# Kernel tuning notes

Measured on AMD Instinct MI355X. Metric: run time of the kernel, lower is better.

The kernel has to match this reference:

```python
import jax, jax.numpy as jnp
import numpy as np

D = 512
H = 8
DH = D // H
FF = 2048
E = 4
EPS = 1e-5


def _layernorm(x, g, b):
    mu = jnp.mean(x, axis=-1, keepdims=True)
    var = jnp.mean(jnp.square(x - mu), axis=-1, keepdims=True)
    return (x - mu) * jax.lax.rsqrt(var + EPS) * g + b


def setup_inputs() -> dict:
    key = jax.random.key(0)
    ks = jax.random.split(key, 12)
    B, T = 4, 2048
    s = 0.02
    return {
        "x": jax.random.normal(ks[0], (B, T, D), jnp.float32),
        "fourier_bias": jax.random.normal(ks[1], (B, T, T), jnp.float32) * 0.1,
        "Wk": jax.random.normal(ks[2], (D, D), jnp.float32) * s,
        "bk": jnp.zeros((D,), jnp.float32),
        "Wv": jax.random.normal(ks[3], (D, D), jnp.float32) * s,
        "bv": jnp.zeros((D,), jnp.float32),
        "Wo": jax.random.normal(ks[4], (D, D), jnp.float32) * s,
        "bo": jnp.zeros((D,), jnp.float32),
        "ln1_g": jnp.ones((D,), jnp.float32),
        "ln1_b": jnp.zeros((D,), jnp.float32),
        "Wg": jax.random.normal(ks[5], (D, E), jnp.float32) * s,
        "bg": jnp.zeros((E,), jnp.float32),
        "W1": jax.random.normal(ks[6], (E, D, FF), jnp.float32) * s,
        "b1": jnp.zeros((E, FF), jnp.float32),
        "W2": jax.random.normal(ks[7], (E, FF, D), jnp.float32) * s,
        "b2": jnp.zeros((E, D), jnp.float32),
        "ln2_g": jnp.ones((D,), jnp.float32),
        "ln2_b": jnp.zeros((D,), jnp.float32),
    }


def reference(x, fourier_bias, Wk, bk, Wv, bv, Wo, bo, ln1_g, ln1_b,
              Wg, bg, W1, b1, W2, b2, ln2_g, ln2_b):
    B, T, _ = x.shape
    # --- Fourier pairwise-bias "attention" ---
    K = (x @ Wk + bk).reshape(B, T, H, DH).transpose(0, 2, 1, 3)  # [B,H,T,Dh]
    V = (x @ Wv + bv).reshape(B, T, H, DH).transpose(0, 2, 1, 3)  # [B,H,T,Dh]
    # sum_j (K_j + fb_ij) * V_j = sum_j K_j*V_j  +  sum_j fb_ij * V_j
    kv_sum = jnp.sum(K * V, axis=2, keepdims=True)                # [B,H,1,Dh]
    fbV = jnp.einsum('bij,bhjd->bhid', fourier_bias, V)           # [B,H,T,Dh]
    wv = (kv_sum + fbV).transpose(0, 2, 1, 3).reshape(B, T, D)
    x = _layernorm(x + (wv @ Wo + bo), ln1_g, ln1_b)
    # --- MoE FFN, top-2 gating (dropout/noise inactive in eval) ---
    scores = jax.nn.softmax(x @ Wg + bg, axis=-1)                 # [B,T,E]
    vals, idx = jax.lax.top_k(scores, 2)                          # [B,T,2]
    w = (jax.nn.one_hot(idx[..., 0], E, dtype=x.dtype) * vals[..., 0:1]
         + jax.nn.one_hot(idx[..., 1], E, dtype=x.dtype) * vals[..., 1:2])  # [B,T,E]
    h = jax.nn.relu(jnp.einsum('btd,edf->btef', x, W1) + b1)      # [B,T,E,FF]
    y = jnp.einsum('btef,efd->bted', h, W2) + b2                  # [B,T,E,D]
    ff = jnp.einsum('bte,bted->btd', w, y)
    return _layernorm(x + ff, ln2_g, ln2_b)
```

## Files before the change

### kernel.cpp

```cpp
#include <hip/hip_runtime.h>
#include <stdint.h>

#define BB   4
#define TT   2048
#define DD   512
#define FFF  2048
#define NEXP 4
#define NTOK (BB*TT)
#define LNEPS 1e-5f

typedef unsigned short u16;
typedef __attribute__((ext_vector_type(8))) short bf16x8;
typedef __attribute__((ext_vector_type(4))) float f32x4;

__device__ __forceinline__ u16 f2bf(float f) {
  union { float f; unsigned u; } v; v.f = f;
  return (u16)((v.u + 0x7FFFu + ((v.u >> 16) & 1u)) >> 16);
}
__device__ __forceinline__ float bf2f(u16 h) {
  union { unsigned u; float f; } v; v.u = (unsigned)h << 16; return v.f;
}

__device__ __forceinline__ void gl2lds(const u16* g, u16* l) {
  __builtin_amdgcn_global_load_lds(
      (const __attribute__((address_space(1))) void*)g,
      (__attribute__((address_space(3))) void*)l, 16, 0, 0);
}


__global__ void split_f32_kernel(const float* __restrict__ in, u16* __restrict__ hi,
                                 u16* __restrict__ lo, int n4) {
  int i = blockIdx.x * blockDim.x + threadIdx.x;
  if (i >= n4) return;
  float4 f = ((const float4*)in)[i];
  u16 h0 = f2bf(f.x), h1 = f2bf(f.y), h2 = f2bf(f.z), h3 = f2bf(f.w);
  u16 l0 = f2bf(f.x - bf2f(h0)), l1 = f2bf(f.y - bf2f(h1));
  u16 l2 = f2bf(f.z - bf2f(h2)), l3 = f2bf(f.w - bf2f(h3));
  ((uint2*)hi)[i] = uint2{(unsigned)h0 | ((unsigned)h1 << 16), (unsigned)h2 | ((unsigned)h3 << 16)};
  ((uint2*)lo)[i] = uint2{(unsigned)l0 | ((unsigned)l1 << 16), (unsigned)l2 | ((unsigned)l3 << 16)};
}

__global__ void transpose_split3_kernel(const float* __restrict__ s0, const float* __restrict__ s1,
                                        const float* __restrict__ s2,
                                        u16* __restrict__ kvhi, u16* __restrict__ kvlo,
                                        u16* __restrict__ ohi,  u16* __restrict__ olo) {
  __shared__ float tile[32][33];
  const int z = blockIdx.z;
  const float* in = (z == 0) ? s0 : (z == 1) ? s1 : s2;
  int c0 = blockIdx.x * 32, r0 = blockIdx.y * 32;
  int tx = threadIdx.x, ty = threadIdx.y;
#pragma unroll
  for (int k = 0; k < 4; k++)
    tile[ty + 8*k][tx] = in[(size_t)(r0 + ty + 8*k) * DD + c0 + tx];
  __syncthreads();
#pragma unroll
  for (int k = 0; k < 4; k++) {
    float v = tile[tx][ty + 8*k];
    u16 h = f2bf(v);
    u16 l = f2bf(v - bf2f(h));
    const int c = c0 + ty + 8*k;
    if (z < 2) {
      size_t idx = (size_t)(2*c + z) * DD + r0 + tx;
      kvhi[idx] = h; kvlo[idx] = l;
    } else {
      size_t idx = (size_t)c * DD + r0 + tx;
      ohi[idx] = h; olo[idx] = l;
    }
  }
}

__global__ void transpose_cast_kernel(const float* __restrict__ in, u16* __restrict__ out,
                                      int R, int C) {
  __shared__ float tile[32][33];
  int z = blockIdx.z;
  in  += (size_t)z * R * C;
  out += (size_t)z * R * C;
  int c0 = blockIdx.x * 32, r0 = blockIdx.y * 32;
  int tx = threadIdx.x, ty = threadIdx.y;
#pragma unroll
  for (int k = 0; k < 4; k++)
    tile[ty + 8*k][tx] = in[(size_t)(r0 + ty + 8*k) * C + c0 + tx];
  __syncthreads();
#pragma unroll
  for (int k = 0; k < 4; k++)
    out[(size_t)(c0 + ty + 8*k) * R + r0 + tx] = f2bf(tile[tx][ty + 8*k]);
}

template<int MODE>
__global__ __launch_bounds__(256)
void gemm_split2_kernel(const u16* __restrict__ Ahi, const u16* __restrict__ Alo,
                        const u16* __restrict__ Bhi, const u16* __restrict__ Blo,
                        const float* __restrict__ bias0, const float* __restrict__ bias1,
                        float* __restrict__ out0,
                        u16* __restrict__ outh, u16* __restrict__ outl,
                        int M, int N, int K,
                        long long sA, long long sB, long long sO) {
  constexpr int NBUF = (MODE == 2) ? 2 : 1;
  __shared__ u16 AhL[NBUF][128*32], AlL[NBUF][128*32];
  __shared__ u16 BhL[NBUF][64*32],  BlL[NBUF][64*32];

  int mt, nt, z;
  if constexpr (MODE == 2) {
    const int gid = blockIdx.x;
    const int xcd = gid & 7, slot = gid >> 3;
    z  = xcd >> 1;
    mt = (xcd & 1) + 2 * (slot >> 3);
    nt = slot & 7;
  } else {
    mt = blockIdx.x; nt = blockIdx.y; z = blockIdx.z;
  }
  const int m0 = mt * 128, n0 = nt * 64;

  Ahi += (size_t)z * sA; Alo += (size_t)z * sA;
  Bhi += (size_t)z * sB; Blo += (size_t)z * sB;
  const int tid = threadIdx.x;
  const int lane = tid & 63, wave = tid >> 6;
  const int wm = wave >> 1, wn = wave & 1;
  const int quad = lane >> 4, l16 = lane & 15;
  const int sxor = ((l16 >> 1) & 3) << 3;

  const int ar1 = tid >> 2;
  const int ac1 = (((tid & 3) ^ ((tid >> 3) & 3)) << 3);
  const u16* pAh1 = Ahi + (size_t)(m0 + ar1) * K + ac1;
  const u16* pAh2 = Ahi + (size_t)(m0 + ar1 + 64) * K + ac1;
  const u16* pAl1 = Alo + (size_t)(m0 + ar1) * K + ac1;
  const u16* pAl2 = Alo + (size_t)(m0 + ar1 + 64) * K + ac1;
  const u16* pBh1 = Bhi + (size_t)(n0 + ar1) * K + ac1;
  const u16* pBl1 = Blo + (size_t)(n0 + ar1) * K + ac1;
  const int wofs = wave * 512;

  f32x4 acc[4][2];
#pragma unroll
  for (int i = 0; i < 4; i++)
#pragma unroll
    for (int j = 0; j < 2; j++)
      acc[i][j] = f32x4{0.f, 0.f, 0.f, 0.f};

  const int NIT = K >> 5;
  if constexpr (MODE == 2) {
    gl2lds(pAh1, &AhL[0][wofs]); gl2lds(pAh2, &AhL[0][2048 + wofs]);
    gl2lds(pAl1, &AlL[0][wofs]); gl2lds(pAl2, &AlL[0][2048 + wofs]);
    gl2lds(pBh1, &BhL[0][wofs]); gl2lds(pBl1, &BlL[0][wofs]);
    for (int it = 0; it < NIT; it++) {
      const int buf = it & 1;
      __syncthreads();
      if (it + 1 < NIT) {
        const int ko = (it + 1) << 5;
        gl2lds(pAh1 + ko, &AhL[buf ^ 1][wofs]); gl2lds(pAh2 + ko, &AhL[buf ^ 1][2048 + wofs]);
        gl2lds(pAl1 + ko, &AlL[buf ^ 1][wofs]); gl2lds(pAl2 + ko, &AlL[buf ^ 1][2048 + wofs]);
        gl2lds(pBh1 + ko, &BhL[buf ^ 1][wofs]); gl2lds(pBl1 + ko, &BlL[buf ^ 1][wofs]);
      }
      bf16x8 afh[4], afl[4], bqh[2], bql[2];
#pragma unroll
      for (int i = 0; i < 4; i++) {
        afh[i] = *(const bf16x8*)&AhL[buf][(wm*64 + i*16 + l16) * 32 + (quad*8 ^ sxor)];
        afl[i] = *(const bf16x8*)&AlL[buf][(wm*64 + i*16 + l16) * 32 + (quad*8 ^ sxor)];
      }
#pragma unroll
      for (int j = 0; j < 2; j++) {
        bqh[j] = *(const bf16x8*)&BhL[buf][(wn*32 + j*16 + l16) * 32 + (quad*8 ^ sxor)];
        bql[j] = *(const bf16x8*)&BlL[buf][(wn*32 + j*16 + l16) * 32 + (quad*8 ^ sxor)];
      }
#pragma unroll
      for (int i = 0; i < 4; i++)
#pragma unroll
        for (int j = 0; j < 2; j++) {
          acc[i][j] = __builtin_amdgcn_mfma_f32_16x16x32_bf16(afh[i], bqh[j], acc[i][j], 0, 0, 0);
          acc[i][j] = __builtin_amdgcn_mfma_f32_16x16x32_bf16(afh[i], bql[j], acc[i][j], 0, 0, 0);
          acc[i][j] = __builtin_amdgcn_mfma_f32_16x16x32_bf16(afl[i], bqh[j], acc[i][j], 0, 0, 0);
        }
    }
  } else {
    for (int it = 0; it < NIT; it++) {
      const int ko = it << 5;
      __syncthreads();
      gl2lds(pAh1 + ko, &AhL[0][wofs]); gl2lds(pAh2 + ko, &AhL[0][2048 + wofs]);
      gl2lds(pAl1 + ko, &AlL[0][wofs]); gl2lds(pAl2 + ko, &AlL[0][2048 + wofs]);
      gl2lds(pBh1 + ko, &BhL[0][wofs]); gl2lds(pBl1 + ko, &BlL[0][wofs]);
      __syncthreads();
      bf16x8 afh[4], afl[4], bqh[2], bql[2];
#pragma unroll
      for (int i = 0; i < 4; i++) {
        afh[i] = *(const bf16x8*)&AhL[0][(wm*64 + i*16 + l16) * 32 + (quad*8 ^ sxor)];
        afl[i] = *(const bf16x8*)&AlL[0][(wm*64 + i*16 + l16) * 32 + (quad*8 ^ sxor)];
      }
#pragma unroll
      for (int j = 0; j < 2; j++) {
        bqh[j] = *(const bf16x8*)&BhL[0][(wn*32 + j*16 + l16) * 32 + (quad*8 ^ sxor)];
        bql[j] = *(const bf16x8*)&BlL[0][(wn*32 + j*16 + l16) * 32 + (quad*8 ^ sxor)];
      }
#pragma unroll
      for (int i = 0; i < 4; i++)
#pragma unroll
        for (int j = 0; j < 2; j++) {
          acc[i][j] = __builtin_amdgcn_mfma_f32_16x16x32_bf16(afh[i], bqh[j], acc[i][j], 0, 0, 0);
          acc[i][j] = __builtin_amdgcn_mfma_f32_16x16x32_bf16(afh[i], bql[j], acc[i][j], 0, 0, 0);
          acc[i][j] = __builtin_amdgcn_mfma_f32_16x16x32_bf16(afl[i], bqh[j], acc[i][j], 0, 0, 0);
        }
    }
  }

  if constexpr (MODE == 1) {
    const int b = m0 >> 11;
    const int rb0 = m0 & (TT - 1);
    const int colbase = n0 + wn*32 + l16;
    float kvp[2] = {0.f, 0.f};
#pragma unroll
    for (int i = 0; i < 4; i++) {
#pragma unroll
      for (int j = 0; j < 2; j++) {
        const int col = colbase + j*16;
        const int d = col >> 1;
        float vals[4];
#pragma unroll
        for (int r = 0; r < 4; r++) {
          float vv = acc[i][j][r] + ((col & 1) ? bias1[d] : bias0[d]);
          float pa = __shfl_xor(vv, 1);
          if (!(col & 1)) kvp[j] += vv * pa;
          vals[r] = vv;
        }
        if (col & 1) {
          const int rr = rb0 + wm*64 + i*16 + quad*4;
          u16 hs[4], ls[4];
#pragma unroll
          for (int r = 0; r < 4; r++) {
            hs[r] = f2bf(vals[r]);
            ls[r] = f2bf(vals[r] - bf2f(hs[r]));
          }
          size_t o = (size_t)b * DD * TT + (size_t)d * TT + rr;
          *(uint2*)&outh[o] = uint2{(unsigned)hs[0] | ((unsigned)hs[1]<<16),
                                    (unsigned)hs[2] | ((unsigned)hs[3]<<16)};
          *(uint2*)&outl[o] = uint2{(unsigned)ls[0] | ((unsigned)ls[1]<<16),
                                    (unsigned)ls[2] | ((unsigned)ls[3]<<16)};
        }
      }
    }
#pragma unroll
    for (int j = 0; j < 2; j++) {
      float p = kvp[j];
      p += __shfl_xor(p, 16);
      p += __shfl_xor(p, 32);
      const int col = colbase + j*16;
      if (!(col & 1) && quad == 0)
        atomicAdd(&out0[b * DD + (col >> 1)], p);
    }
  } else {
#pragma unroll
    for (int i = 0; i < 4; i++) {
#pragma unroll
      for (int r = 0; r < 4; r++) {
        const int row = m0 + wm*64 + i*16 + quad*4 + r;
#pragma unroll
        for (int j = 0; j < 2; j++) {
          const int col = n0 + wn*32 + j*16 + l16;
          float v = acc[i][j][r];
          if constexpr (MODE == 0) {
            out0[(size_t)row * N + col] = v + bias0[col];
          } else {
            v += bias0[(size_t)z * DD + col];
            u16 hv = f2bf(v);
            size_t idx = (size_t)z * sO + (size_t)row * DD + col;
            outh[idx] = hv;
            outl[idx] = f2bf(v - bf2f(hv));
          }
        }
      }
    }
  }
}

__global__ __launch_bounds__(256)
void moe_gemm1_kernel(const u16* __restrict__ X, const int* __restrict__ tokl,
                      const int* __restrict__ cnt, const u16* __restrict__ W1t,
                      const float* __restrict__ b1, u16* __restrict__ H) {
  const int e = blockIdx.z;
  int base = 0, cnte = 0;
#pragma unroll
  for (int i = 0; i < NEXP; i++) { int c = cnt[i]; if (i < e) base += c; if (i == e) cnte = c; }
  const int m0 = blockIdx.x * 128;
  if (m0 >= cnte) return;
  __shared__ u16 As[128*32], Bs[128*32];
  const int n0 = blockIdx.y * 128;
  const int tid = threadIdx.x, lane = tid & 63, wave = tid >> 6;
  const int wm = wave >> 1, wn = wave & 1, quad = lane >> 4, l16 = lane & 15;
  const int sxor = ((l16 >> 1) & 3) << 3;
  const int ar1 = tid >> 2;
  const int ac1 = (((tid & 3) ^ ((tid >> 3) & 3)) << 3);
  const int i1 = m0 + ar1 < cnte ? m0 + ar1 : cnte - 1;
  const int i2 = m0 + ar1 + 64 < cnte ? m0 + ar1 + 64 : cnte - 1;
  const int t1 = tokl[e * NTOK + i1], t2 = tokl[e * NTOK + i2];
  const u16* Bt = W1t + (size_t)e * DD * FFF;
  const float* bias = b1 + (size_t)e * FFF;
  const u16* pA1 = X + (size_t)t1 * DD + ac1;
  const u16* pA2 = X + (size_t)t2 * DD + ac1;
  const u16* pB1 = Bt + (size_t)(n0 + ar1) * DD + ac1;
  const u16* pB2 = Bt + (size_t)(n0 + ar1 + 64) * DD + ac1;
  const int wofs = wave * 512;

  f32x4 acc[4][4];
#pragma unroll
  for (int i = 0; i < 4; i++)
#pragma unroll
    for (int j = 0; j < 4; j++)
      acc[i][j] = f32x4{0.f, 0.f, 0.f, 0.f};

  const int NIT = DD >> 5;
  for (int it = 0; it < NIT; it++) {
    const int ko = it << 5;
    __syncthreads();
    gl2lds(pA1 + ko, &As[wofs]); gl2lds(pA2 + ko, &As[2048 + wofs]);
    gl2lds(pB1 + ko, &Bs[wofs]); gl2lds(pB2 + ko, &Bs[2048 + wofs]);
    __syncthreads();
    bf16x8 af[4], bq[4];
#pragma unroll
    for (int i = 0; i < 4; i++)
      af[i] = *(const bf16x8*)&As[(wm*64 + i*16 + l16)*32 + (quad*8 ^ sxor)];
#pragma unroll
    for (int j = 0; j < 4; j++)
      bq[j] = *(const bf16x8*)&Bs[(wn*64 + j*16 + l16)*32 + (quad*8 ^ sxor)];
#pragma unroll
    for (int i = 0; i < 4; i++)
#pragma unroll
      for (int j = 0; j < 4; j++)
        acc[i][j] = __builtin_amdgcn_mfma_f32_16x16x32_bf16(af[i], bq[j], acc[i][j], 0, 0, 0);
  }

#pragma unroll
  for (int i = 0; i < 4; i++) {
#pragma unroll
    for (int r = 0; r < 4; r++) {
      const int m = m0 + wm*64 + i*16 + quad*4 + r;
      if (m < cnte) {
#pragma unroll
        for (int j = 0; j < 4; j++) {
          const int col = n0 + wn*64 + j*16 + l16;
          H[(size_t)(base + m) * FFF + col] = f2bf(fmaxf(acc[i][j][r] + bias[col], 0.f));
        }
      }
    }
  }
}

__global__ __launch_bounds__(256)
void moe_gemm2_kernel(const u16* __restrict__ H, const int* __restrict__ tokl,
                      const int* __restrict__ cnt, const u16* __restrict__ W2t,
                      const float* __restrict__ b2, const float* __restrict__ wgt,
                      u16* __restrict__ Y) {
  const int e = blockIdx.z;
  int base = 0, cnte = 0;
#pragma unroll
  for (int i = 0; i < NEXP; i++) { int c = cnt[i]; if (i < e) base += c; if (i == e) cnte = c; }
  const int m0 = blockIdx.x * 128;
  if (m0 >= cnte) return;
  __shared__ u16 As[3][128*32], Bs[3][128*32];
  const int n0 = blockIdx.y * 128;
  const int tid = threadIdx.x, lane = tid & 63, wave = tid >> 6;
  const int wm = wave >> 1, wn = wave & 1, quad = lane >> 4, l16 = lane & 15;
  const int sxor = ((l16 >> 1) & 3) << 3;
  const int ar1 = tid >> 2;
  const int ac1 = (((tid & 3) ^ ((tid >> 3) & 3)) << 3);
  const int i1 = m0 + ar1 < cnte ? m0 + ar1 : cnte - 1;
  const int i2 = m0 + ar1 + 64 < cnte ? m0 + ar1 + 64 : cnte - 1;
  const u16* Bt = W2t + (size_t)e * FFF * DD;
  const float* bias = b2 + (size_t)e * DD;
  const u16* pA1 = H + (size_t)(base + i1) * FFF + ac1;
  const u16* pA2 = H + (size_t)(base + i2) * FFF + ac1;
  const u16* pB1 = Bt + (size_t)(n0 + ar1) * FFF + ac1;
  const u16* pB2 = Bt + (size_t)(n0 + ar1 + 64) * FFF + ac1;
  const int wofs = wave * 512;

  f32x4 acc[4][4];
#pragma unroll
  for (int i = 0; i < 4; i++)
#pragma unroll
    for (int j = 0; j < 4; j++)
      acc[i][j] = f32x4{0.f, 0.f, 0.f, 0.f};

  const int NIT = FFF >> 5;
  gl2lds(pA1, &As[0][wofs]); gl2lds(pA2, &As[0][2048 + wofs]);
  gl2lds(pB1, &Bs[0][wofs]); gl2lds(pB2, &Bs[0][2048 + wofs]);
  gl2lds(pA1 + 32, &As[1][wofs]); gl2lds(pA2 + 32, &As[1][2048 + wofs]);
  gl2lds(pB1 + 32, &Bs[1][wofs]); gl2lds(pB2 + 32, &Bs[1][2048 + wofs]);
#pragma unroll 1
  for (int it = 0; it < NIT; it++) {
    const int buf = it % 3;
    if (it < NIT - 1) {
      asm volatile("s_waitcnt vmcnt(4)" ::: "memory");
    } else {
      asm volatile("s_waitcnt vmcnt(0)" ::: "memory");
    }
    __builtin_amdgcn_s_barrier();
    __builtin_amdgcn_sched_barrier(0);
    if (it + 2 < NIT) {
      const int ko = (it + 2) << 5;
      const int pb = (it + 2) % 3;
      gl2lds(pA1 + ko, &As[pb][wofs]); gl2lds(pA2 + ko, &As[pb][2048 + wofs]);
      gl2lds(pB1 + ko, &Bs[pb][wofs]); gl2lds(pB2 + ko, &Bs[pb][2048 + wofs]);
    }
    bf16x8 af[4], bq[4];
#pragma unroll
    for (int i = 0; i < 4; i++)
      af[i] = *(const bf16x8*)&As[buf][(wm*64 + i*16 + l16)*32 + (quad*8 ^ sxor)];
#pragma unroll
    for (int j = 0; j < 4; j++)
      bq[j] = *(const bf16x8*)&Bs[buf][(wn*64 + j*16 + l16)*32 + (quad*8 ^ sxor)];
#pragma unroll
    for (int i = 0; i < 4; i++)
#pragma unroll
      for (int j = 0; j < 4; j++)
        acc[i][j] = __builtin_amdgcn_mfma_f32_16x16x32_bf16(af[i], bq[j], acc[i][j], 0, 0, 0);
  }

#pragma unroll
  for (int i = 0; i < 4; i++) {
#pragma unroll
    for (int r = 0; r < 4; r++) {
      const int m = m0 + wm*64 + i*16 + quad*4 + r;
      if (m < cnte) {
        const int t = tokl[e * NTOK + m];
        const float w = wgt[(size_t)t * NEXP + e];
#pragma unroll
        for (int j = 0; j < 4; j++) {
          const int col = n0 + wn*64 + j*16 + l16;
          Y[(size_t)(base + m) * DD + col] = f2bf((acc[i][j][r] + bias[col]) * w);
        }
      }
    }
  }
}

__global__ void ln_kernel(const float* __restrict__ a, const float* __restrict__ b,
                          const float* __restrict__ g, const float* __restrict__ beta,
                          float* __restrict__ outf, u16* __restrict__ outb) {
  int t = blockIdx.x;
  int tid = threadIdx.x;
  float v0 = a[(size_t)t*DD + tid]       + b[(size_t)t*DD + tid];
  float v1 = a[(size_t)t*DD + 256 + tid] + b[(size_t)t*DD + 256 + tid];
  float s = v0 + v1, s2 = v0*v0 + v1*v1;
  for (int off = 32; off; off >>= 1) { s += __shfl_down(s, off); s2 += __shfl_down(s2, off); }
  __shared__ float ws[4], ws2[4];
  if ((tid & 63) == 0) { ws[tid >> 6] = s; ws2[tid >> 6] = s2; }
  __syncthreads();
  if (tid == 0) {
    float ts = 0, ts2 = 0;
    for (int i = 0; i < 4; i++) { ts += ws[i]; ts2 += ws2[i]; }
    ws[0] = ts; ws2[0] = ts2;
  }
  __syncthreads();
  float mean = ws[0] * (1.f / DD);
  float var  = ws2[0] * (1.f / DD) - mean * mean;
  float rstd = rsqrtf(var + LNEPS);
  float o0 = (v0 - mean) * rstd * g[tid]       + beta[tid];
  float o1 = (v1 - mean) * rstd * g[256 + tid] + beta[256 + tid];
  outf[(size_t)t*DD + tid]       = o0;
  outf[(size_t)t*DD + 256 + tid] = o1;
  outb[(size_t)t*DD + tid]       = f2bf(o0);
  outb[(size_t)t*DD + 256 + tid] = f2bf(o1);
}

__global__ void ln2_kernel(const float* __restrict__ x1, const u16* __restrict__ Y,
                           const int* __restrict__ tokslot, const int* __restrict__ cnt,
                           const float* __restrict__ g, const float* __restrict__ beta,
                           float* __restrict__ out) {
  int t = blockIdx.x;
  int tid = threadIdx.x;
  const int c0 = cnt[0], c1 = cnt[1], c2 = cnt[2];
  const int s0 = tokslot[2*t], s1 = tokslot[2*t + 1];
  const int e0 = s0 >> 14, k0 = s0 & 16383;
  const int e1 = s1 >> 14, k1 = s1 & 16383;
  const int b0 = (e0 > 0 ? c0 : 0) + (e0 > 1 ? c1 : 0) + (e0 > 2 ? c2 : 0);
  const int b1 = (e1 > 0 ? c0 : 0) + (e1 > 1 ? c1 : 0) + (e1 > 2 ? c2 : 0);
  const u16* y0 = Y + (size_t)(b0 + k0) * DD;
  const u16* y1 = Y + (size_t)(b1 + k1) * DD;
  float v0 = x1[(size_t)t*DD + tid]       + bf2f(y0[tid])       + bf2f(y1[tid]);
  float v1 = x1[(size_t)t*DD + 256 + tid] + bf2f(y0[256 + tid]) + bf2f(y1[256 + tid]);
  float s = v0 + v1, s2 = v0*v0 + v1*v1;
  for (int off = 32; off; off >>= 1) { s += __shfl_down(s, off); s2 += __shfl_down(s2, off); }
  __shared__ float ws[4], ws2[4];
  if ((tid & 63) == 0) { ws[tid >> 6] = s; ws2[tid >> 6] = s2; }
  __syncthreads();
  if (tid == 0) {
    float ts = 0, ts2 = 0;
    for (int i = 0; i < 4; i++) { ts += ws[i]; ts2 += ws2[i]; }
    ws[0] = ts; ws2[0] = ts2;
  }
  __syncthreads();
  float mean = ws[0] * (1.f / DD);
  float var  = ws2[0] * (1.f / DD) - mean * mean;
  float rstd = rsqrtf(var + LNEPS);
  out[(size_t)t*DD + tid]       = (v0 - mean) * rstd * g[tid]       + beta[tid];
  out[(size_t)t*DD + 256 + tid] = (v1 - mean) * rstd * g[256 + tid] + beta[256 + tid];
}

__global__ __launch_bounds__(256)
void gate_kernel(const float* __restrict__ x1, const float* __restrict__ Wg,
                 const float* __restrict__ bg, float* __restrict__ wfull,
                 int* __restrict__ tokl, int* __restrict__ cnt, int* __restrict__ tokslot) {
  __shared__ int lcnt[NEXP];
  __shared__ int lbase[NEXP];
  __shared__ int lslots[NEXP][128];
  const int tid = threadIdx.x, lane = tid & 63, wave = tid >> 6;
  if (tid < NEXP) lcnt[tid] = 0;
  __syncthreads();
  const int tblk = blockIdx.x * 64;
  for (int i = 0; i < 16; i++) {
    const int t = tblk + wave * 16 + i;
    float s0 = 0.f, s1 = 0.f, s2 = 0.f, s3 = 0.f;
    for (int d = lane; d < DD; d += 64) {
      float xv = x1[(size_t)t * DD + d];
      float4 w = *(const float4*)&Wg[d * 4];
      s0 += xv * w.x; s1 += xv * w.y; s2 += xv * w.z; s3 += xv * w.w;
    }
    for (int off = 32; off; off >>= 1) {
      s0 += __shfl_down(s0, off); s1 += __shfl_down(s1, off);
      s2 += __shfl_down(s2, off); s3 += __shfl_down(s3, off);
    }
    if (lane == 0) {
      float sc[4] = {s0 + bg[0], s1 + bg[1], s2 + bg[2], s3 + bg[3]};
      float mx = fmaxf(fmaxf(sc[0], sc[1]), fmaxf(sc[2], sc[3]));
      float sum = 0.f;
      for (int e = 0; e < 4; e++) { sc[e] = expf(sc[e] - mx); sum += sc[e]; }
      float inv = 1.f / sum;
      for (int e = 0; e < 4; e++) sc[e] *= inv;
      int i0 = 0;
      for (int e = 1; e < 4; e++) if (sc[e] > sc[i0]) i0 = e;
      int i1 = -1;
      for (int e = 0; e < 4; e++) { if (e == i0) continue; if (i1 < 0 || sc[e] > sc[i1]) i1 = e; }
      float w[4] = {0.f, 0.f, 0.f, 0.f};
      w[i0] = sc[i0]; w[i1] = sc[i1];
      *(float4*)&wfull[(size_t)t * 4] = float4{w[0], w[1], w[2], w[3]};
      int p0 = atomicAdd(&lcnt[i0], 1); lslots[i0][p0] = (t << 1);
      int p1 = atomicAdd(&lcnt[i1], 1); lslots[i1][p1] = (t << 1) | 1;
    }
  }
  __syncthreads();
  if (tid < NEXP) lbase[tid] = atomicAdd(&cnt[tid], lcnt[tid]);
  __syncthreads();
  for (int idx = tid; idx < NEXP * 128; idx += 256) {
    const int e = idx >> 7, p = idx & 127;
    if (p < lcnt[e]) {
      const int v = lslots[e][p];
      const int t = v >> 1;
      const int pos = lbase[e] + p;
      tokl[e * NTOK + pos] = t;
      tokslot[2 * t + (v & 1)] = (e << 14) | pos;
    }
  }
}

extern "C" void kernel_launch(void* const* d_in, const int* in_sizes, int n_in,
                              void* d_out, int out_size, void* d_ws, size_t ws_size,
                              hipStream_t stream) {
  const float* x    = (const float*)d_in[0];
  const float* fb   = (const float*)d_in[1];
  const float* Wk   = (const float*)d_in[2];
  const float* bk   = (const float*)d_in[3];
  const float* Wv   = (const float*)d_in[4];
  const float* bv   = (const float*)d_in[5];
  const float* Wo   = (const float*)d_in[6];
  const float* bo   = (const float*)d_in[7];
  const float* ln1g = (const float*)d_in[8];
  const float* ln1b = (const float*)d_in[9];
  const float* Wg   = (const float*)d_in[10];
  const float* bg   = (const float*)d_in[11];
  const float* W1   = (const float*)d_in[12];
  const float* b1   = (const float*)d_in[13];
  const float* W2   = (const float*)d_in[14];
  const float* b2   = (const float*)d_in[15];
  const float* ln2g = (const float*)d_in[16];
  const float* ln2b = (const float*)d_in[17];

  const size_t MiB = 1048576;
  char* ws = (char*)d_ws;
  char* R1 = ws;
  u16* xhi  = (u16*)R1;             u16* xlo  = (u16*)(R1 + 8*MiB);
  u16* wvhi = (u16*)R1;             u16* wvlo = (u16*)(R1 + 8*MiB);
  u16* x1b  = (u16*)R1;
  char* R2 = ws + 16*MiB;
  u16* fbhi = (u16*)R2;             u16* fblo = (u16*)(R2 + 32*MiB);
  u16* h    = (u16*)R2;
  char* R3 = ws + 80*MiB;
  u16* vthi   = (u16*)R3;           u16* vtlo  = (u16*)(R3 + 8*MiB);
  float* attn = (float*)R3;
  u16*  yb    = (u16*)R3;
  float* x1f  = (float*)(R3 + 16*MiB);
  char* R4 = ws + 112*MiB;
  u16* wkvthi = (u16*)R4;
  u16* wkvtlo = (u16*)(R4 + 1*MiB);
  u16* wothi  = (u16*)(R4 + 2*MiB);
  u16* wotlo  = (u16*)(R4 + 2*MiB + 512*1024);
  u16* w1t    = (u16*)(R4 + 3*MiB);
  u16* w2t    = (u16*)(R4 + 11*MiB);
  char* R5 = ws + 131*MiB;
  float* kvs    = (float*)R5;
  int*   cnt    = (int*)(R5 + 8192);
  float* wfull  = (float*)(R5 + 16*1024);
  int*   tokl   = (int*)(R5 + 160*1024);
  int*   tokslot= (int*)(R5 + 320*1024);
  (void)ws_size; (void)in_sizes; (void)n_in; (void)out_size;

  dim3 tb(32, 8);

  hipMemsetAsync(kvs, 0, 8192 + 16, stream);

  split_f32_kernel<<<NTOK * DD / 4 / 256, 256, 0, stream>>>(x, xhi, xlo, NTOK * DD / 4);
  split_f32_kernel<<<BB * TT * TT / 4 / 256, 256, 0, stream>>>(fb, fbhi, fblo, BB * TT * TT / 4);
  transpose_split3_kernel<<<dim3(16, 16, 3), tb, 0, stream>>>(Wk, Wv, Wo,
                                                              wkvthi, wkvtlo, wothi, wotlo);
  transpose_cast_kernel<<<dim3(FFF/32, DD/32, NEXP), tb, 0, stream>>>(W1, w1t, DD, FFF);
  transpose_cast_kernel<<<dim3(DD/32, FFF/32, NEXP), tb, 0, stream>>>(W2, w2t, FFF, DD);

  gemm_split2_kernel<1><<<dim3(64, 16, 1), 256, 0, stream>>>(
      xhi, xlo, wkvthi, wkvtlo, bk, bv, kvs, vthi, vtlo,
      NTOK, 2*DD, DD, 0, 0, 0);

  gemm_split2_kernel<2><<<dim3(512, 1, 1), 256, 0, stream>>>(
      fbhi, fblo, vthi, vtlo, kvs, nullptr, nullptr, wvhi, wvlo,
      TT, DD, TT, (long long)TT*TT, (long long)DD*TT, (long long)TT*DD);

  gemm_split2_kernel<0><<<dim3(64, 8, 1), 256, 0, stream>>>(
      wvhi, wvlo, wothi, wotlo, bo, nullptr, attn, nullptr, nullptr,
      NTOK, DD, DD, 0, 0, 0);

  ln_kernel<<<NTOK, 256, 0, stream>>>(x, attn, ln1g, ln1b, x1f, x1b);

  gate_kernel<<<NTOK / 64, 256, 0, stream>>>(x1f, Wg, bg, wfull, tokl, cnt, tokslot);

  moe_gemm1_kernel<<<dim3(NTOK/128, FFF/128, NEXP), 256, 0, stream>>>(
      x1b, tokl, cnt, w1t, b1, h);
  moe_gemm2_kernel<<<dim3(NTOK/128, DD/128, NEXP), 256, 0, stream>>>(
      h, tokl, cnt, w2t, b2, wfull, yb);

  ln2_kernel<<<NTOK, 256, 0, stream>>>(x1f, yb, tokslot, cnt, ln2g, ln2b, (float*)d_out);
}
```

Baseline: 508.1 us.

## Triple-buffer LDS tiles in MoE GEMM1 with async prefetch two steps ahead

Turns the single-buffered global-to-LDS load loop in the first MoE expert GEMM into a three-stage ring buffer. Tiles are prefetched two iterations ahead, and each iteration waits on vmcnt and issues a single barrier. This lets global load latency overlap the MFMA compute and drops one of the two syncthreads per K-step. In exchange it triples LDS use, which may lower occupancy, and it depends on correct vmcnt accounting to stay safe.

```diff
diff --git a/kernel.cpp b/kernel.cpp
--- a/kernel.cpp
+++ b/kernel.cpp
@@ -279,7 +279,7 @@
   for (int i = 0; i < NEXP; i++) { int c = cnt[i]; if (i < e) base += c; if (i == e) cnte = c; }
   const int m0 = blockIdx.x * 128;
   if (m0 >= cnte) return;
-  __shared__ u16 As[128*32], Bs[128*32];
+  __shared__ u16 As[3][128*32], Bs[3][128*32];
   const int n0 = blockIdx.y * 128;
   const int tid = threadIdx.x, lane = tid & 63, wave = tid >> 6;
   const int wm = wave >> 1, wn = wave & 1, quad = lane >> 4, l16 = lane & 15;
@@ -305,19 +305,33 @@
       acc[i][j] = f32x4{0.f, 0.f, 0.f, 0.f};
 
   const int NIT = DD >> 5;
+  gl2lds(pA1, &As[0][wofs]); gl2lds(pA2, &As[0][2048 + wofs]);
+  gl2lds(pB1, &Bs[0][wofs]); gl2lds(pB2, &Bs[0][2048 + wofs]);
+  gl2lds(pA1 + 32, &As[1][wofs]); gl2lds(pA2 + 32, &As[1][2048 + wofs]);
+  gl2lds(pB1 + 32, &Bs[1][wofs]); gl2lds(pB2 + 32, &Bs[1][2048 + wofs]);
+#pragma unroll 1
   for (int it = 0; it < NIT; it++) {
-    const int ko = it << 5;
-    __syncthreads();
-    gl2lds(pA1 + ko, &As[wofs]); gl2lds(pA2 + ko, &As[2048 + wofs]);
-    gl2lds(pB1 + ko, &Bs[wofs]); gl2lds(pB2 + ko, &Bs[2048 + wofs]);
-    __syncthreads();
+    const int buf = it % 3;
+    if (it < NIT - 1) {
+      asm volatile("s_waitcnt vmcnt(4)" ::: "memory");
+    } else {
+      asm volatile("s_waitcnt vmcnt(0)" ::: "memory");
+    }
+    __builtin_amdgcn_s_barrier();
+    __builtin_amdgcn_sched_barrier(0);
+    if (it + 2 < NIT) {
+      const int ko = (it + 2) << 5;
+      const int pb = (it + 2) % 3;
+      gl2lds(pA1 + ko, &As[pb][wofs]); gl2lds(pA2 + ko, &As[pb][2048 + wofs]);
+      gl2lds(pB1 + ko, &Bs[pb][wofs]); gl2lds(pB2 + ko, &Bs[pb][2048 + wofs]);
+    }
     bf16x8 af[4], bq[4];
 #pragma unroll
     for (int i = 0; i < 4; i++)
-      af[i] = *(const bf16x8*)&As[(wm*64 + i*16 + l16)*32 + (quad*8 ^ sxor)];
+      af[i] = *(const bf16x8*)&As[buf][(wm*64 + i*16 + l16)*32 + (quad*8 ^ sxor)];
 #pragma unroll
     for (int j = 0; j < 4; j++)
-      bq[j] = *(const bf16x8*)&Bs[(wn*64 + j*16 + l16)*32 + (quad*8 ^ sxor)];
+      bq[j] = *(const bf16x8*)&Bs[buf][(wn*64 + j*16 + l16)*32 + (quad*8 ^ sxor)];
 #pragma unroll
     for (int i = 0; i < 4; i++)
 #pragma unroll
```

Result: no change. 513.3 us (+1.0%).
